# Optimization experiments

Measured on AMD Instinct MI355X. Metric: run time of the kernel, lower is better.

## Reference

```python
import jax, jax.numpy as jnp
import numpy as np

B, N, C, H = 8, 1024, 768, 12
D = C // H
SCALE = D ** -0.5
EPS = 1e-8
LN_EPS = 1e-5


def _layer_norm(x, g, b):
    mu = jnp.mean(x, axis=-1, keepdims=True)
    var = jnp.var(x, axis=-1, keepdims=True)
    return (x - mu) * jax.lax.rsqrt(var + LN_EPS) * g + b


def setup_inputs() -> dict:
    key = jax.random.key(0)
    ks = jax.random.split(key, 8)
    xav_qkv = (2.0 / (C + 3 * C)) ** 0.5 * (3 ** 0.5)  # xavier_uniform bound-ish scale
    xav_p = (2.0 / (C + C)) ** 0.5 * (3 ** 0.5)
    return {
        "x": jax.random.normal(ks[0], (B, N, C), jnp.float32),
        "w_qkv_id": jax.random.uniform(ks[1], (C, 3 * C), jnp.float32, -xav_qkv, xav_qkv),
        "w_qkv_attr": jax.random.uniform(ks[2], (C, 3 * C), jnp.float32, -xav_qkv, xav_qkv),
        "w_proj_id": jax.random.uniform(ks[3], (C, C), jnp.float32, -xav_p, xav_p),
        "b_proj_id": jnp.zeros((C,), jnp.float32),
        "w_proj_attr": jax.random.uniform(ks[4], (C, C), jnp.float32, -xav_p, xav_p),
        "b_proj_attr": jnp.zeros((C,), jnp.float32),
        "ortho_temp": jnp.array(1.0, jnp.float32),
        "ln_id_g": jnp.ones((C,), jnp.float32),
        "ln_id_b": jnp.zeros((C,), jnp.float32),
        "ln_attr_g": jnp.ones((C,), jnp.float32),
        "ln_attr_b": jnp.zeros((C,), jnp.float32),
    }


def _branch_qkv(x, w_qkv):
    # [B,N,3C] -> [3,B,H,N,D]
    qkv = (x @ w_qkv).reshape(B, N, 3, H, D).transpose(2, 0, 3, 1, 4)
    return qkv[0], qkv[1], qkv[2]


def _softmax_attn(q, k):
    scores = jnp.einsum("bhnd,bhmd->bhnm", q, k) * SCALE
    scores = jnp.clip(scores, -20.0, 20.0)
    return jax.nn.softmax(scores, axis=-1)


def reference(x, w_qkv_id, w_qkv_attr, w_proj_id, b_proj_id, w_proj_attr, b_proj_attr,
              ortho_temp, ln_id_g, ln_id_b, ln_attr_g, ln_attr_b):
    q_i, k_i, v_i = _branch_qkv(x, w_qkv_id)
    q_a, k_a, v_a = _branch_qkv(x, w_qkv_attr)
    attn_id = _softmax_attn(q_i, k_i)      # [B,H,N,N]
    attn_attr = _softmax_attn(q_a, k_a)    # [B,H,N,N]

    # soft orthogonal mask: per-row overlap of the two attention distributions
    overlap = ((attn_id + EPS) * (attn_attr + EPS)).sum(axis=-1, keepdims=True)
    temp = jnp.clip(ortho_temp, 0.1, 5.0)
    mask = jax.nn.sigmoid(-overlap * temp)  # same mask for both branches

    def mask_renorm(a):
        am = a * mask
        am = am / (am.sum(axis=-1, keepdims=True) + EPS)
        return jnp.where(jnp.isnan(am), 0.0, am)

    attn_id_m = mask_renorm(attn_id)
    attn_attr_m = mask_renorm(attn_attr)

    out_id = jnp.einsum("bhnm,bhmd->bhnd", attn_id_m, v_i).transpose(0, 2, 1, 3).reshape(B, N, C)
    out_attr = jnp.einsum("bhnm,bhmd->bhnd", attn_attr_m, v_a).transpose(0, 2, 1, 3).reshape(B, N, C)

    id_features = _layer_norm(out_id @ w_proj_id + b_proj_id, ln_id_g, ln_id_b)
    attr_features = _layer_norm(out_attr @ w_proj_attr + b_proj_attr, ln_attr_g, ln_attr_b)
    return (id_features, attr_features)
```

## Files before the change

kernel.cpp:

```cpp
#include <hip/hip_runtime.h>
#include <hip/hip_bf16.h>

#define ASG __attribute__((address_space(1)))
#define ASL __attribute__((address_space(3)))

typedef __attribute__((ext_vector_type(8))) short short8;
typedef __attribute__((ext_vector_type(4))) float f32x4;
typedef unsigned int u32;

__device__ __forceinline__ void gl16(const void* g, void* l) {
  __builtin_amdgcn_global_load_lds((ASG const u32*)g, (ASL u32*)l, 16, 0, 0);
}
__device__ __forceinline__ int swz(int b) { return b ^ (((b >> 7) & 7) << 4); }

union BF4 { ushort4 u; __hip_bfloat16 h[4]; };

__global__ void cvt_x_kernel(const float* __restrict__ x, __hip_bfloat16* __restrict__ xb) {
  int i = (blockIdx.x * 256 + threadIdx.x) * 4;
  float4 f = *(const float4*)(x + i);
  BF4 p;
  p.h[0] = __float2bfloat16(f.x); p.h[1] = __float2bfloat16(f.y);
  p.h[2] = __float2bfloat16(f.z); p.h[3] = __float2bfloat16(f.w);
  *(ushort4*)(xb + i) = p.u;
}

__global__ void tcvt_kernel(const float* __restrict__ src, __hip_bfloat16* __restrict__ dst, int ncols) {
  __shared__ float tile[64][65];
  int n0 = blockIdx.x * 64, k0 = blockIdx.y * 64;
  int t = threadIdx.x;
  int cr = t >> 6, cc = t & 63;
#pragma unroll
  for (int i = 0; i < 16; ++i) {
    int kk = i * 4 + cr;
    tile[kk][cc] = src[(size_t)(k0 + kk) * ncols + n0 + cc];
  }
  __syncthreads();
#pragma unroll
  for (int i = 0; i < 16; ++i) {
    int nn = i * 4 + cr;
    dst[(size_t)(n0 + nn) * 768 + k0 + cc] = __float2bfloat16(tile[cc][nn]);
  }
}

__global__ __launch_bounds__(256, 2) void gemm_qkv_kernel(
    const __hip_bfloat16* __restrict__ A, const __hip_bfloat16* __restrict__ Bt,
    __hip_bfloat16* __restrict__ qq, __hip_bfloat16* __restrict__ kk,
    __hip_bfloat16* __restrict__ vv) {
  __shared__ __attribute__((aligned(128))) char lds[32768];
  char* Al = lds;
  char* Bl = lds + 16384;
  int tid = threadIdx.x, lane = tid & 63, w = tid >> 6;
  int g = lane >> 4, l15 = lane & 15;
  int bn = blockIdx.x, bm = blockIdx.y;
  int wm = w >> 1, wn = w & 1;
  const int LDR = 1536;
  const char* Ab = (const char*)A + (size_t)bm * 128 * LDR;
  const char* Bb = (const char*)Bt + (size_t)bn * 128 * LDR;
  f32x4 zero = {0.f, 0.f, 0.f, 0.f};
  f32x4 acc[4][4];
#pragma unroll
  for (int mt = 0; mt < 4; ++mt)
#pragma unroll
    for (int nt = 0; nt < 4; ++nt) acc[mt][nt] = zero;

  for (int kt = 0; kt < 12; ++kt) {
    __syncthreads();
    const char* As = Ab + kt * 128;
    const char* Bs = Bb + kt * 128;
#pragma unroll
    for (int j = 0; j < 4; ++j) {
      int ci = (w * 4 + j) * 64 + lane;
      int rr = ci >> 3, cc = ci & 7;
      int co = (cc ^ (rr & 7)) << 4;
      gl16(As + (size_t)rr * LDR + co, Al + (w * 4 + j) * 1024);
      gl16(Bs + (size_t)rr * LDR + co, Bl + (w * 4 + j) * 1024);
    }
    __syncthreads();
#pragma unroll
    for (int ks = 0; ks < 2; ++ks) {
      short8 af[4], bf[4];
#pragma unroll
      for (int mt = 0; mt < 4; ++mt)
        af[mt] = *(const short8*)(Al + swz((wm * 64 + mt * 16 + l15) * 128 + ks * 64 + g * 16));
#pragma unroll
      for (int nt = 0; nt < 4; ++nt)
        bf[nt] = *(const short8*)(Bl + swz((wn * 64 + nt * 16 + l15) * 128 + ks * 64 + g * 16));
#pragma unroll
      for (int mt = 0; mt < 4; ++mt)
#pragma unroll
        for (int nt = 0; nt < 4; ++nt)
          acc[mt][nt] = __builtin_amdgcn_mfma_f32_16x16x32_bf16(af[mt], bf[nt], acc[mt][nt], 0, 0, 0);
    }
  }
  int mbase = bm * 128 + wm * 64;
  int nbase = bn * 128 + wn * 64;
#pragma unroll
  for (int mt = 0; mt < 4; ++mt) {
#pragma unroll
    for (int nt = 0; nt < 4; ++nt) {
      int n = nbase + nt * 16 + l15;
      int m0 = mbase + mt * 16 + g * 4;
      int br = (n >= 2304) ? 1 : 0;
      int n3 = n - br * 2304;
      int qkv = n3 / 768;
      int rem = n3 - qkv * 768;
      int h = rem >> 6, d = rem & 63;
      int b = m0 >> 10, ns0 = m0 & 1023;
      size_t bh = (size_t)(br * 8 + b) * 12 + h;
      f32x4 a = acc[mt][nt];
      if (qkv == 0) {
        __hip_bfloat16* dst = qq + bh * 65536 + (size_t)ns0 * 64 + d;
#pragma unroll
        for (int r = 0; r < 4; ++r) dst[r * 64] = __float2bfloat16(a[r]);
      } else if (qkv == 1) {
        __hip_bfloat16* dst = kk + bh * 65536 + (size_t)ns0 * 64 + d;
#pragma unroll
        for (int r = 0; r < 4; ++r) dst[r * 64] = __float2bfloat16(a[r]);
      } else {
        BF4 p;
#pragma unroll
        for (int r = 0; r < 4; ++r) p.h[r] = __float2bfloat16(a[r]);
        *(ushort4*)(vv + bh * 65536 + (size_t)d * 1024 + ns0) = p.u;
      }
    }
  }
}

__global__ __launch_bounds__(256, 2) void attn_kernel(
    const __hip_bfloat16* __restrict__ qarr, const __hip_bfloat16* __restrict__ karr,
    const __hip_bfloat16* __restrict__ varr, __hip_bfloat16* __restrict__ out) {
  __shared__ __attribute__((aligned(128))) char lds[32768];
  char* Ql = lds;
  char* Kl = lds + 8192;
  char* Vl = lds + 16384;
  char* Pl = lds + 24576;
  int tid = threadIdx.x, lane = tid & 63, w = tid >> 6;
  int g = lane >> 4, l15 = lane & 15;
  int qt = blockIdx.x, bh = blockIdx.y, br = blockIdx.z;
  size_t bho = (size_t)(br * 96 + bh);
  const char* qb = (const char*)qarr + bho * 131072 + (size_t)qt * 8192;
  const char* kb = (const char*)karr + bho * 131072;
  const char* vb = (const char*)varr + bho * 131072;

#pragma unroll
  for (int j = 0; j < 2; ++j) {
    int ci = (w * 2 + j) * 64 + lane;
    int rr = ci >> 3, cc = ci & 7;
    gl16(qb + rr * 128 + ((cc ^ (rr & 7)) << 4), Ql + (w * 2 + j) * 1024);
  }
  __syncthreads();
  short8 qf[2];
#pragma unroll
  for (int ks = 0; ks < 2; ++ks)
    qf[ks] = *(const short8*)(Ql + swz((w * 16 + l15) * 128 + ks * 64 + g * 16));

  f32x4 zero = {0.f, 0.f, 0.f, 0.f};
  f32x4 o[4];
#pragma unroll
  for (int dt = 0; dt < 4; ++dt) o[dt] = zero;
  float m[4], l[4];
#pragma unroll
  for (int r = 0; r < 4; ++r) { m[r] = -1e30f; l[r] = 0.f; }

  for (int kt = 0; kt < 16; ++kt) {
    __syncthreads();
#pragma unroll
    for (int j = 0; j < 2; ++j) {
      int ci = (w * 2 + j) * 64 + lane;
      int rr = ci >> 3, cc = ci & 7;
      int co = (cc ^ (rr & 7)) << 4;
      gl16(kb + kt * 8192 + rr * 128 + co, Kl + (w * 2 + j) * 1024);
      gl16(vb + (size_t)rr * 2048 + kt * 128 + co, Vl + (w * 2 + j) * 1024);
    }
    __syncthreads();
    f32x4 s[4];
#pragma unroll
    for (int nt = 0; nt < 4; ++nt) {
      s[nt] = zero;
#pragma unroll
      for (int ks = 0; ks < 2; ++ks) {
        short8 kf = *(const short8*)(Kl + swz((nt * 16 + l15) * 128 + ks * 64 + g * 16));
        s[nt] = __builtin_amdgcn_mfma_f32_16x16x32_bf16(qf[ks], kf, s[nt], 0, 0, 0);
      }
    }
    float p[4][4], tmax[4], tsum[4];
#pragma unroll
    for (int r = 0; r < 4; ++r) {
      float mx = -1e30f;
#pragma unroll
      for (int nt = 0; nt < 4; ++nt) {
        float v = fminf(fmaxf(s[nt][r] * 0.125f, -20.f), 20.f);
        p[nt][r] = v;
        mx = fmaxf(mx, v);
      }
      tmax[r] = mx;
    }
#pragma unroll
    for (int off = 1; off < 16; off <<= 1)
#pragma unroll
      for (int r = 0; r < 4; ++r) tmax[r] = fmaxf(tmax[r], __shfl_xor(tmax[r], off));
    float al[4];
#pragma unroll
    for (int r = 0; r < 4; ++r) {
      float mn = fmaxf(m[r], tmax[r]);
      al[r] = __expf(m[r] - mn);
      m[r] = mn;
    }
#pragma unroll
    for (int r = 0; r < 4; ++r) {
      float su = 0.f;
#pragma unroll
      for (int nt = 0; nt < 4; ++nt) {
        float e = __expf(p[nt][r] - m[r]);
        p[nt][r] = e;
        su += e;
      }
      tsum[r] = su;
    }
#pragma unroll
    for (int off = 1; off < 16; off <<= 1)
#pragma unroll
      for (int r = 0; r < 4; ++r) tsum[r] += __shfl_xor(tsum[r], off);
#pragma unroll
    for (int r = 0; r < 4; ++r) l[r] = l[r] * al[r] + tsum[r];
#pragma unroll
    for (int dt = 0; dt < 4; ++dt)
#pragma unroll
      for (int r = 0; r < 4; ++r) o[dt][r] = o[dt][r] * al[r];
#pragma unroll
    for (int nt = 0; nt < 4; ++nt)
#pragma unroll
      for (int r = 0; r < 4; ++r) {
        int row = w * 16 + g * 4 + r;
        int col = nt * 16 + l15;
        *(__hip_bfloat16*)(Pl + swz(row * 128 + col * 2)) = __float2bfloat16(p[nt][r]);
      }
    asm volatile("s_waitcnt lgkmcnt(0)" ::: "memory");
#pragma unroll
    for (int ks = 0; ks < 2; ++ks) {
      short8 pf = *(const short8*)(Pl + swz((w * 16 + l15) * 128 + ks * 64 + g * 16));
#pragma unroll
      for (int dt = 0; dt < 4; ++dt) {
        short8 vf = *(const short8*)(Vl + swz((dt * 16 + l15) * 128 + ks * 64 + g * 16));
        o[dt] = __builtin_amdgcn_mfma_f32_16x16x32_bf16(pf, vf, o[dt], 0, 0, 0);
      }
    }
  }
  float inv[4];
#pragma unroll
  for (int r = 0; r < 4; ++r) inv[r] = 1.f / l[r];
  int b = bh / 12, h = bh - b * 12;
#pragma unroll
  for (int dt = 0; dt < 4; ++dt)
#pragma unroll
    for (int r = 0; r < 4; ++r) {
      int ns = qt * 64 + w * 16 + g * 4 + r;
      int c = h * 64 + dt * 16 + l15;
      out[((size_t)(br * 8 + b) * 1024 + ns) * 768 + c] = __float2bfloat16(o[dt][r] * inv[r]);
    }
}

__global__ __launch_bounds__(256, 2) void gemm_proj_kernel(
    const __hip_bfloat16* __restrict__ A, const __hip_bfloat16* __restrict__ BtAll,
    const float* __restrict__ bias_id, const float* __restrict__ bias_at,
    float* __restrict__ proj) {
  __shared__ __attribute__((aligned(128))) char lds[32768];
  char* Al = lds;
  char* Bl = lds + 16384;
  int tid = threadIdx.x, lane = tid & 63, w = tid >> 6;
  int g = lane >> 4, l15 = lane & 15;
  int bn = blockIdx.x, bm = blockIdx.y;
  int wm = w >> 1, wn = w & 1;
  int branch = bm >> 6;
  const int LDR = 1536;
  const char* Ab = (const char*)A + (size_t)bm * 128 * LDR;
  const char* Bb = (const char*)BtAll + (size_t)branch * 589824 * 2 + (size_t)bn * 128 * LDR;
  const float* bias = branch ? bias_at : bias_id;
  f32x4 zero = {0.f, 0.f, 0.f, 0.f};
  f32x4 acc[4][4];
#pragma unroll
  for (int mt = 0; mt < 4; ++mt)
#pragma unroll
    for (int nt = 0; nt < 4; ++nt) acc[mt][nt] = zero;

  for (int kt = 0; kt < 12; ++kt) {
    __syncthreads();
    const char* As = Ab + kt * 128;
    const char* Bs = Bb + kt * 128;
#pragma unroll
    for (int j = 0; j < 4; ++j) {
      int ci = (w * 4 + j) * 64 + lane;
      int rr = ci >> 3, cc = ci & 7;
      int co = (cc ^ (rr & 7)) << 4;
      gl16(As + (size_t)rr * LDR + co, Al + (w * 4 + j) * 1024);
      gl16(Bs + (size_t)rr * LDR + co, Bl + (w * 4 + j) * 1024);
    }
    __syncthreads();
#pragma unroll
    for (int ks = 0; ks < 2; ++ks) {
      short8 af[4], bf[4];
#pragma unroll
      for (int mt = 0; mt < 4; ++mt)
        af[mt] = *(const short8*)(Al + swz((wm * 64 + mt * 16 + l15) * 128 + ks * 64 + g * 16));
#pragma unroll
      for (int nt = 0; nt < 4; ++nt)
        bf[nt] = *(const short8*)(Bl + swz((wn * 64 + nt * 16 + l15) * 128 + ks * 64 + g * 16));
#pragma unroll
      for (int mt = 0; mt < 4; ++mt)
#pragma unroll
        for (int nt = 0; nt < 4; ++nt)
          acc[mt][nt] = __builtin_amdgcn_mfma_f32_16x16x32_bf16(af[mt], bf[nt], acc[mt][nt], 0, 0, 0);
    }
  }
  int mbase = bm * 128 + wm * 64;
  int nbase = bn * 128 + wn * 64;
#pragma unroll
  for (int mt = 0; mt < 4; ++mt)
#pragma unroll
    for (int nt = 0; nt < 4; ++nt) {
      int n = nbase + nt * 16 + l15;
      int m0 = mbase + mt * 16 + g * 4;
      float bv = bias[n];
      float* dst = proj + (size_t)m0 * 768 + n;
#pragma unroll
      for (int r = 0; r < 4; ++r) dst[(size_t)r * 768] = acc[mt][nt][r] + bv;
    }
}

__global__ void ln_kernel(const float* __restrict__ proj,
                          const float* __restrict__ g_id, const float* __restrict__ b_id,
                          const float* __restrict__ g_at, const float* __restrict__ b_at,
                          float* __restrict__ out) {
  int row = blockIdx.x * 4 + (threadIdx.x >> 6);
  int lane = threadIdx.x & 63;
  int br = row >> 13, r = row & 8191;
  const float* x = proj + (size_t)row * 768;
  float4 v[3];
  float s = 0.f, sq = 0.f;
#pragma unroll
  for (int p = 0; p < 3; ++p) {
    v[p] = *(const float4*)(x + lane * 4 + p * 256);
    s += v[p].x + v[p].y + v[p].z + v[p].w;
    sq += v[p].x * v[p].x + v[p].y * v[p].y + v[p].z * v[p].z + v[p].w * v[p].w;
  }
#pragma unroll
  for (int off = 32; off; off >>= 1) {
    s += __shfl_xor(s, off);
    sq += __shfl_xor(sq, off);
  }
  float mean = s * (1.f / 768.f);
  float var = fmaxf(sq * (1.f / 768.f) - mean * mean, 0.f);
  float rstd = rsqrtf(var + 1e-5f);
  const float* gv = br ? g_at : g_id;
  const float* bv = br ? b_at : b_id;
  float* o = out + (size_t)br * 6291456 + (size_t)r * 768;
#pragma unroll
  for (int p = 0; p < 3; ++p) {
    int c = lane * 4 + p * 256;
    float4 ov;
    ov.x = (v[p].x - mean) * rstd * gv[c + 0] + bv[c + 0];
    ov.y = (v[p].y - mean) * rstd * gv[c + 1] + bv[c + 1];
    ov.z = (v[p].z - mean) * rstd * gv[c + 2] + bv[c + 2];
    ov.w = (v[p].w - mean) * rstd * gv[c + 3] + bv[c + 3];
    *(float4*)(o + c) = ov;
  }
}

extern "C" void kernel_launch(void* const* d_in, const int* in_sizes, int n_in,
                              void* d_out, int out_size, void* d_ws, size_t ws_size,
                              hipStream_t stream) {
  const float* x = (const float*)d_in[0];
  const float* w_qkv_id = (const float*)d_in[1];
  const float* w_qkv_attr = (const float*)d_in[2];
  const float* w_proj_id = (const float*)d_in[3];
  const float* b_proj_id = (const float*)d_in[4];
  const float* w_proj_attr = (const float*)d_in[5];
  const float* b_proj_attr = (const float*)d_in[6];
  const float* ln_id_g = (const float*)d_in[8];
  const float* ln_id_b = (const float*)d_in[9];
  const float* ln_attr_g = (const float*)d_in[10];
  const float* ln_attr_b = (const float*)d_in[11];

  char* ws = (char*)d_ws;
  __hip_bfloat16* xb = (__hip_bfloat16*)(ws);
  __hip_bfloat16* wqkvT = (__hip_bfloat16*)(ws + 12582912);
  __hip_bfloat16* wpT = (__hip_bfloat16*)(ws + 19660800);
  __hip_bfloat16* qq = (__hip_bfloat16*)(ws + 22020096);
  __hip_bfloat16* kk = qq + 12582912;
  __hip_bfloat16* vv = kk + 12582912;
  __hip_bfloat16* aout = (__hip_bfloat16*)(ws + 97517568);
  float* proj = (float*)(ws + 22020096);
  float* out = (float*)d_out;

  cvt_x_kernel<<<6144, 256, 0, stream>>>(x, xb);
  tcvt_kernel<<<dim3(36, 12), 256, 0, stream>>>(w_qkv_id, wqkvT, 2304);
  tcvt_kernel<<<dim3(36, 12), 256, 0, stream>>>(w_qkv_attr, wqkvT + (size_t)2304 * 768, 2304);
  tcvt_kernel<<<dim3(12, 12), 256, 0, stream>>>(w_proj_id, wpT, 768);
  tcvt_kernel<<<dim3(12, 12), 256, 0, stream>>>(w_proj_attr, wpT + 589824, 768);
  gemm_qkv_kernel<<<dim3(36, 64), 256, 0, stream>>>(xb, wqkvT, qq, kk, vv);
  attn_kernel<<<dim3(16, 96, 2), 256, 0, stream>>>(qq, kk, vv, aout);
  gemm_proj_kernel<<<dim3(6, 128), 256, 0, stream>>>(aout, wpT, b_proj_id, b_proj_attr, proj);
  ln_kernel<<<4096, 256, 0, stream>>>(proj, ln_id_g, ln_id_b, ln_attr_g, ln_attr_b, out);
}
```

Measured before the change: 395.4 us.

## Restructure attention kernel with 32x32 MFMA, double-buffered K/V, and register-resident P

Rewrites the flash-attention kernel to use 512-thread blocks covering 256 query rows. It computes S^T with 32x32x16 bf16 MFMA so that P stays in registers and is fed directly as the A operand, removing the LDS round-trip for P. K/V tiles are double-buffered with async global-to-LDS loads, so each iteration needs one barrier instead of two. Softmax is moved to the exp2 domain with a pre-scaled clip, and the rescale is skipped lazily when the max grows by no more than 8. Q is now loaded directly from global memory into registers. The risks are higher register pressure with launch_bounds(512,2) and fewer blocks in the grid.

```diff
diff --git a/kernel.cpp b/kernel.cpp
--- a/kernel.cpp
+++ b/kernel.cpp
@@ -4,8 +4,10 @@
 #define ASG __attribute__((address_space(1)))
 #define ASL __attribute__((address_space(3)))
 
+typedef __attribute__((ext_vector_type(4))) short s16x4;
 typedef __attribute__((ext_vector_type(8))) short short8;
 typedef __attribute__((ext_vector_type(4))) float f32x4;
+typedef __attribute__((ext_vector_type(16))) float f32x16;
 typedef unsigned int u32;
 
 __device__ __forceinline__ void gl16(const void* g, void* l) {
@@ -14,6 +16,13 @@
 __device__ __forceinline__ int swz(int b) { return b ^ (((b >> 7) & 7) << 4); }
 
 union BF4 { ushort4 u; __hip_bfloat16 h[4]; };
+
+__device__ __forceinline__ u32 pk2(float lo, float hi) {
+  union { u32 u; __hip_bfloat16 h[2]; } p;
+  p.h[0] = __float2bfloat16(lo);
+  p.h[1] = __float2bfloat16(hi);
+  return p.u;
+}
 
 __global__ void cvt_x_kernel(const float* __restrict__ x, __hip_bfloat16* __restrict__ xb) {
   int i = (blockIdx.x * 256 + threadIdx.x) * 4;
@@ -126,138 +135,139 @@
   }
 }
 
-__global__ __launch_bounds__(256, 2) void attn_kernel(
+union V8 { s16x4 ab[2]; short8 s8; };
+__device__ __forceinline__ short8 ldv(const char* V, int row, int t, int hi) {
+  int off = row * 128 + t * 32 + hi * 8;
+  V8 u;
+  u.ab[0] = *(const s16x4*)(V + swz(off));
+  u.ab[1] = *(const s16x4*)(V + swz(off + 16));
+  return u.s8;
+}
+
+__global__ __launch_bounds__(512, 2) void attn_kernel(
     const __hip_bfloat16* __restrict__ qarr, const __hip_bfloat16* __restrict__ karr,
     const __hip_bfloat16* __restrict__ varr, __hip_bfloat16* __restrict__ out) {
   __shared__ __attribute__((aligned(128))) char lds[32768];
-  char* Ql = lds;
-  char* Kl = lds + 8192;
-  char* Vl = lds + 16384;
-  char* Pl = lds + 24576;
+  char* Kb0 = lds;
+  char* Vb0 = lds + 8192;
+  char* Kb1 = lds + 16384;
+  char* Vb1 = lds + 24576;
   int tid = threadIdx.x, lane = tid & 63, w = tid >> 6;
-  int g = lane >> 4, l15 = lane & 15;
+  int hi = lane >> 5, l31 = lane & 31;
   int qt = blockIdx.x, bh = blockIdx.y, br = blockIdx.z;
   size_t bho = (size_t)(br * 96 + bh);
-  const char* qb = (const char*)qarr + bho * 131072 + (size_t)qt * 8192;
+  const char* qb = (const char*)qarr + bho * 131072;
   const char* kb = (const char*)karr + bho * 131072;
   const char* vb = (const char*)varr + bho * 131072;
 
-#pragma unroll
-  for (int j = 0; j < 2; ++j) {
-    int ci = (w * 2 + j) * 64 + lane;
-    int rr = ci >> 3, cc = ci & 7;
-    gl16(qb + rr * 128 + ((cc ^ (rr & 7)) << 4), Ql + (w * 2 + j) * 1024);
-  }
+  short8 qf[4];
+  const char* qrow = qb + (size_t)(qt * 256 + w * 32 + l31) * 128;
+#pragma unroll
+  for (int ks = 0; ks < 4; ++ks) qf[ks] = *(const short8*)(qrow + ks * 32 + hi * 16);
+
+  int rr = tid >> 3, cc = tid & 7;
+  int co = (cc ^ (rr & 7)) << 4;
+  const char* ksrc = kb + rr * 128 + co;
+  const char* vsrc = vb + rr * 2048 + co;
+  gl16(ksrc, Kb0 + w * 1024);
+  gl16(vsrc, Vb0 + w * 1024);
+
+  f32x16 o0, o1;
+#pragma unroll
+  for (int i = 0; i < 16; ++i) { o0[i] = 0.f; o1[i] = 0.f; }
+  float m = -1e30f, lsum = 0.f;
+  const float SCL = 0.18033688f;
+  const float CL = 28.8539008f;
   __syncthreads();
-  short8 qf[2];
-#pragma unroll
-  for (int ks = 0; ks < 2; ++ks)
-    qf[ks] = *(const short8*)(Ql + swz((w * 16 + l15) * 128 + ks * 64 + g * 16));
-
-  f32x4 zero = {0.f, 0.f, 0.f, 0.f};
-  f32x4 o[4];
-#pragma unroll
-  for (int dt = 0; dt < 4; ++dt) o[dt] = zero;
-  float m[4], l[4];
-#pragma unroll
-  for (int r = 0; r < 4; ++r) { m[r] = -1e30f; l[r] = 0.f; }
 
   for (int kt = 0; kt < 16; ++kt) {
+    char* K = (kt & 1) ? Kb1 : Kb0;
+    char* V = (kt & 1) ? Vb1 : Vb0;
+    if (kt < 15) {
+      char* Kn = (kt & 1) ? Kb0 : Kb1;
+      char* Vn = (kt & 1) ? Vb0 : Vb1;
+      gl16(ksrc + (kt + 1) * 8192, Kn + w * 1024);
+      gl16(vsrc + (kt + 1) * 128, Vn + w * 1024);
+    }
+    f32x16 s0, s1;
+#pragma unroll
+    for (int i = 0; i < 16; ++i) { s0[i] = 0.f; s1[i] = 0.f; }
+    __builtin_amdgcn_s_setprio(1);
+#pragma unroll
+    for (int ks = 0; ks < 4; ++ks) {
+      short8 k0 = *(const short8*)(K + swz(l31 * 128 + ks * 32 + hi * 16));
+      short8 k1 = *(const short8*)(K + swz((32 + l31) * 128 + ks * 32 + hi * 16));
+      s0 = __builtin_amdgcn_mfma_f32_32x32x16_bf16(k0, qf[ks], s0, 0, 0, 0);
+      s1 = __builtin_amdgcn_mfma_f32_32x32x16_bf16(k1, qf[ks], s1, 0, 0, 0);
+    }
+    __builtin_amdgcn_s_setprio(0);
+#pragma unroll
+    for (int i = 0; i < 16; ++i) {
+      s0[i] = fminf(fmaxf(s0[i] * SCL, -CL), CL);
+      s1[i] = fminf(fmaxf(s1[i] * SCL, -CL), CL);
+    }
+    float mx[8];
+#pragma unroll
+    for (int i = 0; i < 8; ++i)
+      mx[i] = fmaxf(fmaxf(s0[i], s0[i + 8]), fmaxf(s1[i], s1[i + 8]));
+    float pm = fmaxf(fmaxf(fmaxf(mx[0], mx[1]), fmaxf(mx[2], mx[3])),
+                     fmaxf(fmaxf(mx[4], mx[5]), fmaxf(mx[6], mx[7])));
+    float rm = fmaxf(pm, __shfl_xor(pm, 32));
+    if (!__all(rm <= m + 8.f)) {
+      float mn = fmaxf(m, rm);
+      float al = exp2f(m - mn);
+      m = mn;
+      lsum *= al;
+#pragma unroll
+      for (int r = 0; r < 16; ++r) {
+        float a = __shfl(al, (r & 3) + 8 * (r >> 2) + 4 * hi);
+        o0[r] *= a;
+        o1[r] *= a;
+      }
+    }
+#pragma unroll
+    for (int i = 0; i < 16; ++i) {
+      s0[i] = exp2f(s0[i] - m);
+      s1[i] = exp2f(s1[i] - m);
+    }
+    float sm[8];
+#pragma unroll
+    for (int i = 0; i < 8; ++i) sm[i] = (s0[i] + s0[i + 8]) + (s1[i] + s1[i + 8]);
+    lsum += ((sm[0] + sm[1]) + (sm[2] + sm[3])) + ((sm[4] + sm[5]) + (sm[6] + sm[7]));
+
+    union PU { u32 u[4]; short8 s8; } pA0, pB0, pA1, pB1;
+#pragma unroll
+    for (int t = 0; t < 4; ++t) {
+      pA0.u[t] = pk2(s0[2 * t], s0[2 * t + 1]);
+      pB0.u[t] = pk2(s0[8 + 2 * t], s0[9 + 2 * t]);
+      pA1.u[t] = pk2(s1[2 * t], s1[2 * t + 1]);
+      pB1.u[t] = pk2(s1[8 + 2 * t], s1[9 + 2 * t]);
+    }
+    __builtin_amdgcn_s_setprio(1);
+    o0 = __builtin_amdgcn_mfma_f32_32x32x16_bf16(pA0.s8, ldv(V, l31, 0, hi), o0, 0, 0, 0);
+    o0 = __builtin_amdgcn_mfma_f32_32x32x16_bf16(pB0.s8, ldv(V, l31, 1, hi), o0, 0, 0, 0);
+    o0 = __builtin_amdgcn_mfma_f32_32x32x16_bf16(pA1.s8, ldv(V, l31, 2, hi), o0, 0, 0, 0);
+    o0 = __builtin_amdgcn_mfma_f32_32x32x16_bf16(pB1.s8, ldv(V, l31, 3, hi), o0, 0, 0, 0);
+    o1 = __builtin_amdgcn_mfma_f32_32x32x16_bf16(pA0.s8, ldv(V, 32 + l31, 0, hi), o1, 0, 0, 0);
+    o1 = __builtin_amdgcn_mfma_f32_32x32x16_bf16(pB0.s8, ldv(V, 32 + l31, 1, hi), o1, 0, 0, 0);
+    o1 = __builtin_amdgcn_mfma_f32_32x32x16_bf16(pA1.s8, ldv(V, 32 + l31, 2, hi), o1, 0, 0, 0);
+    o1 = __builtin_amdgcn_mfma_f32_32x32x16_bf16(pB1.s8, ldv(V, 32 + l31, 3, hi), o1, 0, 0, 0);
+    __builtin_amdgcn_s_setprio(0);
     __syncthreads();
-#pragma unroll
-    for (int j = 0; j < 2; ++j) {
-      int ci = (w * 2 + j) * 64 + lane;
-      int rr = ci >> 3, cc = ci & 7;
-      int co = (cc ^ (rr & 7)) << 4;
-      gl16(kb + kt * 8192 + rr * 128 + co, Kl + (w * 2 + j) * 1024);
-      gl16(vb + (size_t)rr * 2048 + kt * 128 + co, Vl + (w * 2 + j) * 1024);
-    }
-    __syncthreads();
-    f32x4 s[4];
-#pragma unroll
-    for (int nt = 0; nt < 4; ++nt) {
-      s[nt] = zero;
-#pragma unroll
-      for (int ks = 0; ks < 2; ++ks) {
-        short8 kf = *(const short8*)(Kl + swz((nt * 16 + l15) * 128 + ks * 64 + g * 16));
-        s[nt] = __builtin_amdgcn_mfma_f32_16x16x32_bf16(qf[ks], kf, s[nt], 0, 0, 0);
-      }
-    }
-    float p[4][4], tmax[4], tsum[4];
-#pragma unroll
-    for (int r = 0; r < 4; ++r) {
-      float mx = -1e30f;
-#pragma unroll
-      for (int nt = 0; nt < 4; ++nt) {
-        float v = fminf(fmaxf(s[nt][r] * 0.125f, -20.f), 20.f);
-        p[nt][r] = v;
-        mx = fmaxf(mx, v);
-      }
-      tmax[r] = mx;
-    }
-#pragma unroll
-    for (int off = 1; off < 16; off <<= 1)
-#pragma unroll
-      for (int r = 0; r < 4; ++r) tmax[r] = fmaxf(tmax[r], __shfl_xor(tmax[r], off));
-    float al[4];
-#pragma unroll
-    for (int r = 0; r < 4; ++r) {
-      float mn = fmaxf(m[r], tmax[r]);
-      al[r] = __expf(m[r] - mn);
-      m[r] = mn;
-    }
-#pragma unroll
-    for (int r = 0; r < 4; ++r) {
-      float su = 0.f;
-#pragma unroll
-      for (int nt = 0; nt < 4; ++nt) {
-        float e = __expf(p[nt][r] - m[r]);
-        p[nt][r] = e;
-        su += e;
-      }
-      tsum[r] = su;
-    }
-#pragma unroll
-    for (int off = 1; off < 16; off <<= 1)
-#pragma unroll
-      for (int r = 0; r < 4; ++r) tsum[r] += __shfl_xor(tsum[r], off);
-#pragma unroll
-    for (int r = 0; r < 4; ++r) l[r] = l[r] * al[r] + tsum[r];
-#pragma unroll
-    for (int dt = 0; dt < 4; ++dt)
-#pragma unroll
-      for (int r = 0; r < 4; ++r) o[dt][r] = o[dt][r] * al[r];
-#pragma unroll
-    for (int nt = 0; nt < 4; ++nt)
-#pragma unroll
-      for (int r = 0; r < 4; ++r) {
-        int row = w * 16 + g * 4 + r;
-        int col = nt * 16 + l15;
-        *(__hip_bfloat16*)(Pl + swz(row * 128 + col * 2)) = __float2bfloat16(p[nt][r]);
-      }
-    asm volatile("s_waitcnt lgkmcnt(0)" ::: "memory");
-#pragma unroll
-    for (int ks = 0; ks < 2; ++ks) {
-      short8 pf = *(const short8*)(Pl + swz((w * 16 + l15) * 128 + ks * 64 + g * 16));
-#pragma unroll
-      for (int dt = 0; dt < 4; ++dt) {
-        short8 vf = *(const short8*)(Vl + swz((dt * 16 + l15) * 128 + ks * 64 + g * 16));
-        o[dt] = __builtin_amdgcn_mfma_f32_16x16x32_bf16(pf, vf, o[dt], 0, 0, 0);
-      }
-    }
-  }
-  float inv[4];
-#pragma unroll
-  for (int r = 0; r < 4; ++r) inv[r] = 1.f / l[r];
+  }
+
+  float lt = lsum + __shfl_xor(lsum, 32);
+  float linv = 1.f / lt;
   int b = bh / 12, h = bh - b * 12;
-#pragma unroll
-  for (int dt = 0; dt < 4; ++dt)
-#pragma unroll
-    for (int r = 0; r < 4; ++r) {
-      int ns = qt * 64 + w * 16 + g * 4 + r;
-      int c = h * 64 + dt * 16 + l15;
-      out[((size_t)(br * 8 + b) * 1024 + ns) * 768 + c] = __float2bfloat16(o[dt][r] * inv[r]);
-    }
+  size_t rowbase = (size_t)(br * 8 + b) * 1024 + qt * 256 + w * 32;
+#pragma unroll
+  for (int r = 0; r < 16; ++r) {
+    int qr = (r & 3) + 8 * (r >> 2) + 4 * hi;
+    float li = __shfl(linv, qr);
+    __hip_bfloat16* dst = out + (rowbase + qr) * 768 + h * 64 + l31;
+    dst[0] = __float2bfloat16(o0[r] * li);
+    dst[32] = __float2bfloat16(o1[r] * li);
+  }
 }
 
 __global__ __launch_bounds__(256, 2) void gemm_proj_kernel(
@@ -398,7 +408,7 @@
   tcvt_kernel<<<dim3(12, 12), 256, 0, stream>>>(w_proj_id, wpT, 768);
   tcvt_kernel<<<dim3(12, 12), 256, 0, stream>>>(w_proj_attr, wpT + 589824, 768);
   gemm_qkv_kernel<<<dim3(36, 64), 256, 0, stream>>>(xb, wqkvT, qq, kk, vv);
-  attn_kernel<<<dim3(16, 96, 2), 256, 0, stream>>>(qq, kk, vv, aout);
+  attn_kernel<<<dim3(4, 96, 2), 512, 0, stream>>>(qq, kk, vv, aout);
   gemm_proj_kernel<<<dim3(6, 128), 256, 0, stream>>>(aout, wpT, b_proj_id, b_proj_attr, proj);
   ln_kernel<<<4096, 256, 0, stream>>>(proj, ln_id_g, ln_id_b, ln_attr_g, ln_attr_b, out);
 }
```

After: 357.8 us. -9.5%, faster.
